# Kernel optimization log

Measured on AMD Instinct MI355X. Metric: run time of the kernel, lower is better.

## Reference

```python
import jax, jax.numpy as jnp
import numpy as np

D = 12  # grid size per axis (self.shape = [12,12,12])
BN_EPS = 1e-5


def _scatter(feats, idx, B):
    # feats: [N, C], idx: [N, 4] = (b, z, y, x). Coords are unique -> .set is exact.
    g = jnp.zeros((B, D, D, D, feats.shape[-1]), feats.dtype)
    return g.at[idx[:, 0], idx[:, 1], idx[:, 2], idx[:, 3]].set(feats)


def _subm_conv_bn_relu(feats, idx, B, W, b, gamma, beta):
    # Submanifold 3x3x3 conv == dense SAME conv on zero-filled grid, restricted
    # to the active sites (inactive neighbors contribute zero features).
    g = _scatter(feats, idx, B)  # [B, D, D, D, Cin]
    y = jax.lax.conv_general_dilated(
        g, W, window_strides=(1, 1, 1), padding='SAME',
        dimension_numbers=('NDHWC', 'DHWIO', 'NDHWC')) + b
    f = y[idx[:, 0], idx[:, 1], idx[:, 2], idx[:, 3]]  # gather active -> [N, Cout]
    # BatchNorm1d (training mode): biased batch stats over the N active points.
    mu = f.mean(axis=0)
    var = f.var(axis=0)
    f = (f - mu) * jax.lax.rsqrt(var + BN_EPS) * gamma + beta
    return jax.nn.relu(f)


def setup_inputs() -> dict:
    key = jax.random.key(0)
    B, per, Cin = 512, 864, 16
    N = B * per
    k_feat, k_coord, kp = jax.random.split(key, 3)
    # unique active voxels per batch element
    pkeys = jax.random.split(k_coord, B)
    lin = jax.vmap(lambda k: jax.random.permutation(k, D * D * D))(pkeys)[:, :per]  # [B, per]
    z, y, x = lin // (D * D), (lin // D) % D, lin % D
    bids = jnp.broadcast_to(jnp.arange(B)[:, None], (B, per))
    indices = jnp.stack([bids, z, y, x], axis=-1).reshape(N, 4).astype(jnp.int32)
    features = jax.random.normal(k_feat, (N, Cin), dtype=jnp.float32)
    ks = jax.random.split(kp, 6)
    inp = {
        'features': features, 'indices': indices, 'batch_size': B,
        'W0': jax.random.normal(ks[0], (3, 3, 3, Cin, 64), jnp.float32) * 0.05,
        'b0': jax.random.normal(ks[1], (64,), jnp.float32) * 0.05,
        'gamma0': jnp.ones((64,), jnp.float32), 'beta0': jnp.zeros((64,), jnp.float32),
        'W1': jax.random.normal(ks[2], (3, 3, 3, 64, 128), jnp.float32) * 0.05,
        'b1': jax.random.normal(ks[3], (128,), jnp.float32) * 0.05,
        'gamma1': jnp.ones((128,), jnp.float32), 'beta1': jnp.zeros((128,), jnp.float32),
        'W2': jax.random.normal(ks[4], (3, 3, 3, 128, 64), jnp.float32) * 0.05,
        'b2': jax.random.normal(ks[5], (64,), jnp.float32) * 0.05,
        'gamma2': jnp.ones((64,), jnp.float32), 'beta2': jnp.zeros((64,), jnp.float32),
    }
    return inp


def reference(features, indices, batch_size, W0, b0, gamma0, beta0,
              W1, b1, gamma1, beta1, W2, b2, gamma2, beta2):
    B = int(batch_size)
    f = _subm_conv_bn_relu(features, indices, B, W0, b0, gamma0, beta0)
    f = _subm_conv_bn_relu(f, indices, B, W1, b1, gamma1, beta1)
    f = _subm_conv_bn_relu(f, indices, B, W2, b2, gamma2, beta2)
    g = _scatter(f, indices, B)                 # [B, D, D, D, Cout]
    return jnp.transpose(g, (0, 4, 1, 2, 3))    # spconv .dense(): [B, C, D, H, W]
```

## Files before the change

kernel.cpp:

```cpp
#include <hip/hip_runtime.h>

#define DD 12
#define VOX 1728
#define BN_EPS 1e-5f
#define BATCH 512
#define PER 864
#define PERZ 865
#define NTOT (BATCH * PER)

typedef __attribute__((ext_vector_type(8))) short short8;
typedef __attribute__((ext_vector_type(4))) float f32x4;
typedef unsigned short u16;

__device__ inline u16 f2b(float f) {
    union { float f; unsigned u; } v; v.f = f;
    unsigned r = v.u + 0x7fffu + ((v.u >> 16) & 1u);
    return (u16)(r >> 16);
}
__device__ inline float b2f(u16 h) {
    union { unsigned u; float f; } v; v.u = ((unsigned)h) << 16;
    return v.f;
}
constexpr int ilog2(int v) { return v == 1 ? 0 : 1 + ilog2(v / 2); }

__device__ __forceinline__ void async_copy16(const void* g, void* l) {
    __builtin_amdgcn_global_load_lds(
        (const __attribute__((address_space(1))) void*)g,
        (__attribute__((address_space(3))) void*)l, 16, 0, 0);
}

template<int N> __device__ __forceinline__ void wait_vm() {
    if constexpr (N == 0)       asm volatile("s_waitcnt vmcnt(0)"  ::: "memory");
    else if constexpr (N == 8)  asm volatile("s_waitcnt vmcnt(8)"  ::: "memory");
    else if constexpr (N == 10) asm volatile("s_waitcnt vmcnt(10)" ::: "memory");
    else if constexpr (N == 12) asm volatile("s_waitcnt vmcnt(12)" ::: "memory");
    else if constexpr (N == 18) asm volatile("s_waitcnt vmcnt(18)" ::: "memory");
    else static_assert(N == 0, "unhandled vmcnt value");
}

__global__ void build_map_kernel(const int* __restrict__ idx, int* __restrict__ map, int N) {
    int p = blockIdx.x * blockDim.x + threadIdx.x;
    if (p >= N) return;
    const int4 v = ((const int4*)idx)[p];
    map[v.x * VOX + (v.y * DD + v.z) * DD + v.w] = p;
}

__global__ void build_nbr_kernel(const int* __restrict__ idx, const int* __restrict__ map,
                                 u16* __restrict__ nbr, int N) {
    int p = blockIdx.x * blockDim.x + threadIdx.x;
    if (p >= N) return;
    const int4 v = ((const int4*)idx)[p];
    const int base = v.x * VOX;
    const int lb = v.x * PER;
    #pragma unroll
    for (int nk = 0; nk < 27; nk++) {
        int dz = nk / 9 - 1, dy = (nk / 3) % 3 - 1, dx = nk % 3 - 1;
        int zz = v.y + dz, yy = v.z + dy, xx = v.w + dx;
        u16 out = PER;
        if (zz >= 0 && zz < DD && yy >= 0 && yy < DD && xx >= 0 && xx < DD) {
            int q = map[base + (zz * DD + yy) * DD + xx];
            if (q >= 0) out = (u16)(q - lb);
        }
        nbr[nk * N + p] = out;
    }
    #pragma unroll
    for (int nk = 27; nk < 32; nk++) nbr[nk * N + p] = PER;
}

__global__ void transpose_w_kernel(const float* __restrict__ W, u16* __restrict__ Wt,
                                   int K, int COUT, int Kpad) {
    int i = blockIdx.x * blockDim.x + threadIdx.x;
    if (i >= K * COUT) return;
    int n = i % COUT, k = i / COUT;
    Wt[(size_t)n * Kpad + k] = f2b(W[i]);
}

__global__ void zero_rows_kernel(u16* __restrict__ f, int CIN) {
    int t = blockIdx.x * blockDim.x + threadIdx.x;
    int e4 = CIN >> 2;
    if (t >= BATCH * e4) return;
    int b = t / e4, k = t - b * e4;
    ((ushort4*)f)[(size_t)(b * PERZ + PER) * e4 + k] = make_ushort4(0, 0, 0, 0);
}

__global__ void cast_bf16_kernel(const float* __restrict__ in, u16* __restrict__ out, int N4) {
    int i = blockIdx.x * blockDim.x + threadIdx.x;
    if (i >= N4) return;
    float4 v = ((const float4*)in)[i];
    int p = i >> 2, c4 = i & 3;
    int b = p / PER, r = p - b * PER;
    ushort4 o;
    o.x = f2b(v.x); o.y = f2b(v.y); o.z = f2b(v.z); o.w = f2b(v.w);
    ((ushort4*)out)[(size_t)(b * PERZ + r) * 4 + c4] = o;
}

template<int CIN, int COUT, int BM, int WM, int WN>
__global__ __launch_bounds__(256) void conv_mfma_kernel(
    const u16* __restrict__ fin,
    const u16* __restrict__ nbr,
    const u16* __restrict__ Wt,
    const float* __restrict__ bias,
    float* __restrict__ y,
    float* __restrict__ stats) {
    constexpr int Kpad   = (27 * CIN + 63) & ~63;
    constexpr int KSTEPS = Kpad / 64;
    constexpr int L2C    = ilog2(CIN);
    constexpr int BN     = WN * 64;
    constexpr int ASLOTS = BM / 32;
    constexpr int BSLOTS = BN / 32;
    constexpr int A_OFF  = BN * 128;
    constexpr int BUFB   = (BM + BN) * 128;
    static_assert(KSTEPS >= 3, "pipeline prologue needs >=3 K-steps");
    __shared__ char smem[2 * BUFB];

    const int perx = gridDim.x >> 3;
    const int bid = (blockIdx.x & 7) * perx + (blockIdx.x >> 3);
    const int p0 = bid * BM;

    const int tid = threadIdx.x;
    const int wave = tid >> 6, lane = tid & 63;
    const int wm = wave / WN, wn = wave % WN;
    const int lq = lane >> 4, lr = lane & 15;
    const int lrow = lane >> 3;
    const int kc_d = (lane & 7) ^ (lrow & 7);

    int qvoff[ASLOTS], gbase[ASLOTS];
    #pragma unroll
    for (int i = 0; i < ASLOTS; i++) {
        int m = (wave * ASLOTS + i) * 8 + lrow;
        int p = p0 + m;
        int b = p / PER;
        qvoff[i] = (((kc_d * 8) >> L2C) * NTOT + p) * 2;
        gbase[i] = b * PERZ * CIN + ((kc_d * 8) & (CIN - 1));
    }
    int bvoff[BSLOTS];
    #pragma unroll
    for (int j = 0; j < BSLOTS; j++)
        bvoff[j] = ((wave * BSLOTS + j) * 8 + lrow) * Kpad + kc_d * 8;

    int phs[2];
    phs[0] = ((0 + lq) ^ (lr & 7)) * 16;
    phs[1] = ((4 + lq) ^ (lr & 7)) * 16;
    const int aBase = A_OFF + (wm * 64 + lr) * 128;
    const int bBase = (wn * 64 + lr) * 128;

    const f32x4 fzero = {0.f, 0.f, 0.f, 0.f};
    f32x4 acc[4][4];
    #pragma unroll
    for (int i = 0; i < 4; i++)
        #pragma unroll
        for (int j = 0; j < 4; j++) acc[i][j] = fzero;

    u16 q[ASLOTS];
    auto loadQ = [&](int step) {
        int sQ = ((step * 64) >> L2C) * (NTOT * 2);
        #pragma unroll
        for (int i = 0; i < ASLOTS; i++)
            q[i] = *(const u16*)((const char*)nbr + qvoff[i] + sQ);
    };
    auto stage = [&](int step, int bo) {
        int sG = (step * 64) & (CIN - 1);
        const u16* fs = fin + sG;
        #pragma unroll
        for (int i = 0; i < ASLOTS; i++)
            async_copy16(fs + gbase[i] + ((int)q[i] << L2C),
                         smem + bo + A_OFF + (wave * ASLOTS + i) * 1024);
        const u16* wsrc = Wt + step * 64;
        #pragma unroll
        for (int j = 0; j < BSLOTS; j++)
            async_copy16(wsrc + bvoff[j], smem + bo + (wave * BSLOTS + j) * 1024);
    };

    loadQ(0);
    stage(0, 0);
    loadQ(1);

    #pragma unroll 1
    for (int kb = 0; kb < KSTEPS; kb++) {
        if (kb + 1 < KSTEPS) {
            stage(kb + 1, ((kb + 1) & 1) * BUFB);
            if (kb + 2 < KSTEPS) {
                loadQ(kb + 2);
                wait_vm<2 * ASLOTS + BSLOTS>();
            } else {
                wait_vm<ASLOTS + BSLOTS>();
            }
        } else {
            wait_vm<0>();
        }
        __builtin_amdgcn_s_barrier();

        const int so = (kb & 1) * BUFB;
        #pragma unroll
        for (int s = 0; s < 2; s++) {
            short8 af[4], bfr[4];
            #pragma unroll
            for (int i = 0; i < 4; i++)
                af[i] = *(const short8*)(smem + so + aBase + i * 2048 + phs[s]);
            #pragma unroll
            for (int j = 0; j < 4; j++)
                bfr[j] = *(const short8*)(smem + so + bBase + j * 2048 + phs[s]);
            #pragma unroll
            for (int i = 0; i < 4; i++)
                #pragma unroll
                for (int j = 0; j < 4; j++)
                    acc[i][j] = __builtin_amdgcn_mfma_f32_16x16x32_bf16(af[i], bfr[j], acc[i][j], 0, 0, 0);
        }
        asm volatile("s_waitcnt lgkmcnt(0)" ::: "memory");
        __builtin_amdgcn_s_barrier();
    }

    #pragma unroll
    for (int j = 0; j < 4; j++) {
        int col = wn * 64 + j * 16 + lr;
        float bv = bias[col];
        float s = 0.f, s2 = 0.f;
        #pragma unroll
        for (int i = 0; i < 4; i++) {
            int row0 = p0 + wm * 64 + i * 16 + lq * 4;
            #pragma unroll
            for (int r = 0; r < 4; r++) {
                float v = acc[i][j][r] + bv;
                y[(size_t)(row0 + r) * COUT + col] = v;
                s += v; s2 += v * v;
            }
        }
        s  += __shfl_down(s, 32);  s  += __shfl_down(s, 16);
        s2 += __shfl_down(s2, 32); s2 += __shfl_down(s2, 16);
        if (lane < 16) {
            atomicAdd(&stats[col], s);
            atomicAdd(&stats[COUT + col], s2);
        }
    }
}

template<int COUT>
__global__ void finalize_kernel(const float* __restrict__ stats, const float* __restrict__ gamma,
                                const float* __restrict__ beta, float* __restrict__ ss, int N) {
    int co = threadIdx.x;
    float inv_n = 1.f / (float)N;
    float mu  = stats[co] * inv_n;
    float var = stats[COUT + co] * inv_n - mu * mu;
    float sc  = gamma[co] * rsqrtf(var + BN_EPS);
    ss[co]        = sc;
    ss[COUT + co] = beta[co] - mu * sc;
}

template<int COUT>
__global__ void apply_kernel(const float* __restrict__ y, const float* __restrict__ ss,
                             u16* __restrict__ f, int total4) {
    int i = blockIdx.x * blockDim.x + threadIdx.x;
    if (i >= total4) return;
    constexpr int E4 = COUT / 4;
    float4 v = ((const float4*)y)[i];
    int p = i / E4, k = i - p * E4;
    int c0 = k * 4;
    int b = p / PER, r = p - b * PER;
    ushort4 o;
    float a;
    a = fmaf(v.x, ss[c0 + 0], ss[COUT + c0 + 0]); o.x = f2b(a > 0.f ? a : 0.f);
    a = fmaf(v.y, ss[c0 + 1], ss[COUT + c0 + 1]); o.y = f2b(a > 0.f ? a : 0.f);
    a = fmaf(v.z, ss[c0 + 2], ss[COUT + c0 + 2]); o.z = f2b(a > 0.f ? a : 0.f);
    a = fmaf(v.w, ss[c0 + 3], ss[COUT + c0 + 3]); o.w = f2b(a > 0.f ? a : 0.f);
    ((ushort4*)f)[(size_t)(b * PERZ + r) * E4 + k] = o;
}

__global__ void output_kernel(const u16* __restrict__ f, const int* __restrict__ map,
                              float* __restrict__ out, int total) {
    int i = blockIdx.x * blockDim.x + threadIdx.x;
    if (i >= total) return;
    int voxel = i % VOX;
    int bc    = i / VOX;
    int c = bc & 63;
    int b = bc >> 6;
    int p = map[b * VOX + voxel];
    float v = 0.f;
    if (p >= 0) {
        int r = p - b * PER;
        v = b2f(f[(size_t)(b * PERZ + r) * 64 + c]);
    }
    out[i] = v;
}

extern "C" void kernel_launch(void* const* d_in, const int* in_sizes, int n_in,
                              void* d_out, int out_size, void* d_ws, size_t ws_size,
                              hipStream_t stream) {
    const float* feats = (const float*)d_in[0];
    const int*   idx   = (const int*)  d_in[1];
    const float* W0 = (const float*)d_in[3];
    const float* b0 = (const float*)d_in[4];
    const float* g0 = (const float*)d_in[5];
    const float* e0 = (const float*)d_in[6];
    const float* W1 = (const float*)d_in[7];
    const float* b1 = (const float*)d_in[8];
    const float* g1 = (const float*)d_in[9];
    const float* e1 = (const float*)d_in[10];
    const float* W2 = (const float*)d_in[11];
    const float* b2 = (const float*)d_in[12];
    const float* g2 = (const float*)d_in[13];
    const float* e2 = (const float*)d_in[14];

    const int N = in_sizes[0] / 16;

    char* ws = (char*)d_ws;
    size_t off = 0;
    auto alloc = [&](size_t bytes) { void* p = ws + off; off = (off + bytes + 255) & ~(size_t)255; return p; };
    int*   map   = (int*)  alloc((size_t)BATCH * VOX * 4);
    float* stats = (float*)alloc(3 * 256 * 4);
    float* ss    = (float*)alloc(3 * 256 * 4);
    u16*   nbr   = (u16*)  alloc((size_t)N * 32 * 2);
    u16*   wt0   = (u16*)  alloc((size_t)64  * 448  * 2);
    u16*   wt1   = (u16*)  alloc((size_t)128 * 1728 * 2);
    u16*   wt2   = (u16*)  alloc((size_t)64  * 3456 * 2);
    u16*   fbuf  = (u16*)  alloc((size_t)BATCH * PERZ * 128 * 2);
    float* y = (float*)d_out;

    hipMemsetAsync(map,   0xFF, (size_t)BATCH * VOX * 4, stream);
    hipMemsetAsync(stats, 0,    3 * 256 * 4, stream);
    hipMemsetAsync(wt0,   0,    (size_t)64 * 448 * 2, stream);
    build_map_kernel<<<(N + 255) / 256, 256, 0, stream>>>(idx, map, N);
    build_nbr_kernel<<<(N + 255) / 256, 256, 0, stream>>>(idx, map, nbr, N);
    transpose_w_kernel<<<(432  * 64  + 255) / 256, 256, 0, stream>>>(W0, wt0, 432,  64,  448);
    transpose_w_kernel<<<(1728 * 128 + 255) / 256, 256, 0, stream>>>(W1, wt1, 1728, 128, 1728);
    transpose_w_kernel<<<(3456 * 64  + 255) / 256, 256, 0, stream>>>(W2, wt2, 3456, 64,  3456);

    zero_rows_kernel<<<(BATCH * 4 + 255) / 256, 256, 0, stream>>>(fbuf, 16);
    cast_bf16_kernel<<<(N * 4 + 255) / 256, 256, 0, stream>>>(feats, fbuf, N * 4);
    conv_mfma_kernel<16, 64, 256, 4, 1><<<N / 256, 256, 0, stream>>>(fbuf, nbr, wt0, b0, y, stats + 0);
    finalize_kernel<64><<<1, 64, 0, stream>>>(stats + 0, g0, e0, ss + 0, N);
    zero_rows_kernel<<<(BATCH * 16 + 255) / 256, 256, 0, stream>>>(fbuf, 64);
    apply_kernel<64><<<(N * 16 + 255) / 256, 256, 0, stream>>>(y, ss + 0, fbuf, N * 16);

    conv_mfma_kernel<64, 128, 128, 2, 2><<<N / 128, 256, 0, stream>>>(fbuf, nbr, wt1, b1, y, stats + 256);
    finalize_kernel<128><<<1, 128, 0, stream>>>(stats + 256, g1, e1, ss + 256, N);
    zero_rows_kernel<<<(BATCH * 32 + 255) / 256, 256, 0, stream>>>(fbuf, 128);
    apply_kernel<128><<<(N * 32 + 255) / 256, 256, 0, stream>>>(y, ss + 256, fbuf, N * 32);

    conv_mfma_kernel<128, 64, 256, 4, 1><<<N / 256, 256, 0, stream>>>(fbuf, nbr, wt2, b2, y, stats + 512);
    finalize_kernel<64><<<1, 64, 0, stream>>>(stats + 512, g2, e2, ss + 512, N);
    zero_rows_kernel<<<(BATCH * 16 + 255) / 256, 256, 0, stream>>>(fbuf, 64);
    apply_kernel<64><<<(N * 16 + 255) / 256, 256, 0, stream>>>(y, ss + 512, fbuf, N * 16);

    output_kernel<<<(out_size + 255) / 256, 256, 0, stream>>>(fbuf, map, (float*)d_out, out_size);
}
```

Before: 1.358 ms.

## Load weight fragments directly into registers from pre-packed MFMA layout, skipping LDS

Weights are pre-packed into a layout where each lane's MFMA B fragment is one contiguous 16-byte load. The conv kernel now reads B straight from global memory (L2-resident) into double-buffered registers instead of staging it through LDS. This halves LDS traffic and shrinks the shared memory footprint, which may raise occupancy. The cost is more VGPRs (16 short8 buffers) and more in-flight vector memory ops that each step has to wait on.

After: 1.561 ms. 1.15x slower.

```diff
diff --git a/kernel.cpp b/kernel.cpp
--- a/kernel.cpp
+++ b/kernel.cpp
@@ -31,10 +31,9 @@
 
 template<int N> __device__ __forceinline__ void wait_vm() {
     if constexpr (N == 0)       asm volatile("s_waitcnt vmcnt(0)"  ::: "memory");
-    else if constexpr (N == 8)  asm volatile("s_waitcnt vmcnt(8)"  ::: "memory");
-    else if constexpr (N == 10) asm volatile("s_waitcnt vmcnt(10)" ::: "memory");
     else if constexpr (N == 12) asm volatile("s_waitcnt vmcnt(12)" ::: "memory");
-    else if constexpr (N == 18) asm volatile("s_waitcnt vmcnt(18)" ::: "memory");
+    else if constexpr (N == 16) asm volatile("s_waitcnt vmcnt(16)" ::: "memory");
+    else if constexpr (N == 24) asm volatile("s_waitcnt vmcnt(24)" ::: "memory");
     else static_assert(N == 0, "unhandled vmcnt value");
 }
 
@@ -67,12 +66,28 @@
     for (int nk = 27; nk < 32; nk++) nbr[nk * N + p] = PER;
 }
 
-__global__ void transpose_w_kernel(const float* __restrict__ W, u16* __restrict__ Wt,
-                                   int K, int COUT, int Kpad) {
-    int i = blockIdx.x * blockDim.x + threadIdx.x;
-    if (i >= K * COUT) return;
-    int n = i % COUT, k = i / COUT;
-    Wt[(size_t)n * Kpad + k] = f2b(W[i]);
+template<int CIN, int COUT>
+__global__ void pack_w_kernel(const float* __restrict__ W, u16* __restrict__ Wp) {
+    constexpr int K = 27 * CIN;
+    constexpr int KSTEPS = ((K + 63) & ~63) / 64;
+    constexpr int NG = COUT / 64;
+    int t = blockIdx.x * blockDim.x + threadIdx.x;
+    if (t >= KSTEPS * NG * 8 * 64) return;
+    int lane = t & 63;
+    int sj   = (t >> 6) & 7;
+    int gg   = t >> 9;
+    int g = gg % NG, step = gg / NG;
+    int col = g * 64 + (sj & 3) * 16 + (lane & 15);
+    int k0  = step * 64 + (sj >> 2) * 32 + (lane >> 4) * 8;
+    short8 o;
+    #pragma unroll
+    for (int e = 0; e < 8; e++) {
+        int k = k0 + e;
+        u16 val = 0;
+        if (k < K) val = f2b(W[(size_t)k * COUT + col]);
+        ((u16*)&o)[e] = val;
+    }
+    *(short8*)(Wp + (size_t)t * 8) = o;
 }
 
 __global__ void zero_rows_kernel(u16* __restrict__ f, int CIN) {
@@ -98,18 +113,16 @@
 __global__ __launch_bounds__(256) void conv_mfma_kernel(
     const u16* __restrict__ fin,
     const u16* __restrict__ nbr,
-    const u16* __restrict__ Wt,
+    const u16* __restrict__ Wp,
     const float* __restrict__ bias,
     float* __restrict__ y,
     float* __restrict__ stats) {
     constexpr int Kpad   = (27 * CIN + 63) & ~63;
     constexpr int KSTEPS = Kpad / 64;
     constexpr int L2C    = ilog2(CIN);
-    constexpr int BN     = WN * 64;
+    constexpr int NG     = COUT / 64;
     constexpr int ASLOTS = BM / 32;
-    constexpr int BSLOTS = BN / 32;
-    constexpr int A_OFF  = BN * 128;
-    constexpr int BUFB   = (BM + BN) * 128;
+    constexpr int BUFB   = BM * 128;
     static_assert(KSTEPS >= 3, "pipeline prologue needs >=3 K-steps");
     __shared__ char smem[2 * BUFB];
 
@@ -133,16 +146,11 @@
         qvoff[i] = (((kc_d * 8) >> L2C) * NTOT + p) * 2;
         gbase[i] = b * PERZ * CIN + ((kc_d * 8) & (CIN - 1));
     }
-    int bvoff[BSLOTS];
-    #pragma unroll
-    for (int j = 0; j < BSLOTS; j++)
-        bvoff[j] = ((wave * BSLOTS + j) * 8 + lrow) * Kpad + kc_d * 8;
 
     int phs[2];
     phs[0] = ((0 + lq) ^ (lr & 7)) * 16;
     phs[1] = ((4 + lq) ^ (lr & 7)) * 16;
-    const int aBase = A_OFF + (wm * 64 + lr) * 128;
-    const int bBase = (wn * 64 + lr) * 128;
+    const int aBase = (wm * 64 + lr) * 128;
 
     const f32x4 fzero = {0.f, 0.f, 0.f, 0.f};
     f32x4 acc[4][4];
@@ -164,50 +172,60 @@
         #pragma unroll
         for (int i = 0; i < ASLOTS; i++)
             async_copy16(fs + gbase[i] + ((int)q[i] << L2C),
-                         smem + bo + A_OFF + (wave * ASLOTS + i) * 1024);
-        const u16* wsrc = Wt + step * 64;
-        #pragma unroll
-        for (int j = 0; j < BSLOTS; j++)
-            async_copy16(wsrc + bvoff[j], smem + bo + (wave * BSLOTS + j) * 1024);
-    };
-
-    loadQ(0);
-    stage(0, 0);
-    loadQ(1);
-
-    #pragma unroll 1
-    for (int kb = 0; kb < KSTEPS; kb++) {
-        if (kb + 1 < KSTEPS) {
-            stage(kb + 1, ((kb + 1) & 1) * BUFB);
-            if (kb + 2 < KSTEPS) {
-                loadQ(kb + 2);
-                wait_vm<2 * ASLOTS + BSLOTS>();
-            } else {
-                wait_vm<ASLOTS + BSLOTS>();
-            }
-        } else {
-            wait_vm<0>();
-        }
-        __builtin_amdgcn_s_barrier();
-
-        const int so = (kb & 1) * BUFB;
+                         smem + bo + (wave * ASLOTS + i) * 1024);
+    };
+    const char* wpB = (const char*)Wp + (size_t)wn * 8 * 1024 + (size_t)lane * 16;
+    auto loadB = [&](int step, short8 (&bb)[8]) {
+        const char* src = wpB + (size_t)step * (NG * 8 * 1024);
+        #pragma unroll
+        for (int sj = 0; sj < 8; sj++)
+            bb[sj] = *(const short8*)(src + sj * 1024);
+    };
+    auto compute = [&](const short8 (&bb)[8], int so) {
         #pragma unroll
         for (int s = 0; s < 2; s++) {
-            short8 af[4], bfr[4];
+            short8 af[4];
             #pragma unroll
             for (int i = 0; i < 4; i++)
                 af[i] = *(const short8*)(smem + so + aBase + i * 2048 + phs[s]);
             #pragma unroll
-            for (int j = 0; j < 4; j++)
-                bfr[j] = *(const short8*)(smem + so + bBase + j * 2048 + phs[s]);
-            #pragma unroll
             for (int i = 0; i < 4; i++)
                 #pragma unroll
                 for (int j = 0; j < 4; j++)
-                    acc[i][j] = __builtin_amdgcn_mfma_f32_16x16x32_bf16(af[i], bfr[j], acc[i][j], 0, 0, 0);
-        }
+                    acc[i][j] = __builtin_amdgcn_mfma_f32_16x16x32_bf16(af[i], bb[s * 4 + j], acc[i][j], 0, 0, 0);
+        }
+    };
+
+    auto step_body = [&](int kb, short8 (&bC)[8], short8 (&bN)[8]) {
+        if (kb + 1 < KSTEPS) {
+            stage(kb + 1, ((kb + 1) & 1) * BUFB);
+            loadB(kb + 1, bN);
+            if (kb + 2 < KSTEPS) {
+                loadQ(kb + 2);
+                wait_vm<2 * ASLOTS + 8>();
+            } else {
+                wait_vm<ASLOTS + 8>();
+            }
+        } else {
+            wait_vm<0>();
+        }
+        __builtin_amdgcn_s_barrier();
+        compute(bC, (kb & 1) * BUFB);
         asm volatile("s_waitcnt lgkmcnt(0)" ::: "memory");
         __builtin_amdgcn_s_barrier();
+    };
+
+    short8 bX[8], bY[8];
+    loadQ(0);
+    stage(0, 0);
+    loadB(0, bX);
+    loadQ(1);
+
+    #pragma unroll 1
+    for (int kb = 0; kb < KSTEPS; kb += 2) {
+        step_body(kb, bX, bY);
+        if (kb + 1 < KSTEPS)
+            step_body(kb + 1, bY, bX);
     }
 
     #pragma unroll
@@ -309,20 +327,19 @@
     float* stats = (float*)alloc(3 * 256 * 4);
     float* ss    = (float*)alloc(3 * 256 * 4);
     u16*   nbr   = (u16*)  alloc((size_t)N * 32 * 2);
-    u16*   wt0   = (u16*)  alloc((size_t)64  * 448  * 2);
-    u16*   wt1   = (u16*)  alloc((size_t)128 * 1728 * 2);
-    u16*   wt2   = (u16*)  alloc((size_t)64  * 3456 * 2);
+    u16*   wt0   = (u16*)  alloc((size_t)7  * 1 * 512 * 16);
+    u16*   wt1   = (u16*)  alloc((size_t)27 * 2 * 512 * 16);
+    u16*   wt2   = (u16*)  alloc((size_t)54 * 1 * 512 * 16);
     u16*   fbuf  = (u16*)  alloc((size_t)BATCH * PERZ * 128 * 2);
     float* y = (float*)d_out;
 
     hipMemsetAsync(map,   0xFF, (size_t)BATCH * VOX * 4, stream);
     hipMemsetAsync(stats, 0,    3 * 256 * 4, stream);
-    hipMemsetAsync(wt0,   0,    (size_t)64 * 448 * 2, stream);
     build_map_kernel<<<(N + 255) / 256, 256, 0, stream>>>(idx, map, N);
     build_nbr_kernel<<<(N + 255) / 256, 256, 0, stream>>>(idx, map, nbr, N);
-    transpose_w_kernel<<<(432  * 64  + 255) / 256, 256, 0, stream>>>(W0, wt0, 432,  64,  448);
-    transpose_w_kernel<<<(1728 * 128 + 255) / 256, 256, 0, stream>>>(W1, wt1, 1728, 128, 1728);
-    transpose_w_kernel<<<(3456 * 64  + 255) / 256, 256, 0, stream>>>(W2, wt2, 3456, 64,  3456);
+    pack_w_kernel<16,  64 ><<<(7  * 1 * 512 + 255) / 256, 256, 0, stream>>>(W0, wt0);
+    pack_w_kernel<64,  128><<<(27 * 2 * 512 + 255) / 256, 256, 0, stream>>>(W1, wt1);
+    pack_w_kernel<128, 64 ><<<(54 * 1 * 512 + 255) / 256, 256, 0, stream>>>(W2, wt2);
 
     zero_rows_kernel<<<(BATCH * 4 + 255) / 256, 256, 0, stream>>>(fbuf, 16);
     cast_bf16_kernel<<<(N * 4 + 255) / 256, 256, 0, stream>>>(feats, fbuf, N * 4);
```

## Fuse final BN/ReLU into dense output scatter and fold zero-row padding into cast/apply

Applied to the files above, without the earlier changes.

Removes the separate zero_rows launches by having the cast and apply kernels cover padded rows and write zeros there. Conv priority is raised around the MFMA block with s_setprio. When the workspace allows, the last conv writes to a separate buffer and a new fused kernel applies BN+ReLU while transposing through shared memory into the dense NCDHW output. This skips the final bf16 round trip and the strided output gather, at the cost of extra workspace and a fallback path.

Measured after the change: 1.193 ms. -12.1%, faster.

```diff
diff --git a/kernel.cpp b/kernel.cpp
--- a/kernel.cpp
+++ b/kernel.cpp
@@ -75,23 +75,17 @@
     Wt[(size_t)n * Kpad + k] = f2b(W[i]);
 }
 
-__global__ void zero_rows_kernel(u16* __restrict__ f, int CIN) {
-    int t = blockIdx.x * blockDim.x + threadIdx.x;
-    int e4 = CIN >> 2;
-    if (t >= BATCH * e4) return;
-    int b = t / e4, k = t - b * e4;
-    ((ushort4*)f)[(size_t)(b * PERZ + PER) * e4 + k] = make_ushort4(0, 0, 0, 0);
-}
-
-__global__ void cast_bf16_kernel(const float* __restrict__ in, u16* __restrict__ out, int N4) {
+__global__ void cast_bf16_kernel(const float* __restrict__ in, u16* __restrict__ out, int total4) {
     int i = blockIdx.x * blockDim.x + threadIdx.x;
-    if (i >= N4) return;
-    float4 v = ((const float4*)in)[i];
+    if (i >= total4) return;
     int p = i >> 2, c4 = i & 3;
-    int b = p / PER, r = p - b * PER;
-    ushort4 o;
-    o.x = f2b(v.x); o.y = f2b(v.y); o.z = f2b(v.z); o.w = f2b(v.w);
-    ((ushort4*)out)[(size_t)(b * PERZ + r) * 4 + c4] = o;
+    int b = p / PERZ, r = p - b * PERZ;
+    ushort4 o = make_ushort4(0, 0, 0, 0);
+    if (r < PER) {
+        float4 v = ((const float4*)in)[(size_t)(b * PER + r) * 4 + c4];
+        o.x = f2b(v.x); o.y = f2b(v.y); o.z = f2b(v.z); o.w = f2b(v.w);
+    }
+    ((ushort4*)out)[i] = o;
 }
 
 template<int CIN, int COUT, int BM, int WM, int WN>
@@ -191,6 +185,7 @@
         __builtin_amdgcn_s_barrier();
 
         const int so = (kb & 1) * BUFB;
+        __builtin_amdgcn_s_setprio(1);
         #pragma unroll
         for (int s = 0; s < 2; s++) {
             short8 af[4], bfr[4];
@@ -206,6 +201,7 @@
                 for (int j = 0; j < 4; j++)
                     acc[i][j] = __builtin_amdgcn_mfma_f32_16x16x32_bf16(af[i], bfr[j], acc[i][j], 0, 0, 0);
         }
+        __builtin_amdgcn_s_setprio(0);
         asm volatile("s_waitcnt lgkmcnt(0)" ::: "memory");
         __builtin_amdgcn_s_barrier();
     }
@@ -252,17 +248,19 @@
     int i = blockIdx.x * blockDim.x + threadIdx.x;
     if (i >= total4) return;
     constexpr int E4 = COUT / 4;
-    float4 v = ((const float4*)y)[i];
     int p = i / E4, k = i - p * E4;
-    int c0 = k * 4;
-    int b = p / PER, r = p - b * PER;
-    ushort4 o;
-    float a;
-    a = fmaf(v.x, ss[c0 + 0], ss[COUT + c0 + 0]); o.x = f2b(a > 0.f ? a : 0.f);
-    a = fmaf(v.y, ss[c0 + 1], ss[COUT + c0 + 1]); o.y = f2b(a > 0.f ? a : 0.f);
-    a = fmaf(v.z, ss[c0 + 2], ss[COUT + c0 + 2]); o.z = f2b(a > 0.f ? a : 0.f);
-    a = fmaf(v.w, ss[c0 + 3], ss[COUT + c0 + 3]); o.w = f2b(a > 0.f ? a : 0.f);
-    ((ushort4*)f)[(size_t)(b * PERZ + r) * E4 + k] = o;
+    int b = p / PERZ, r = p - b * PERZ;
+    ushort4 o = make_ushort4(0, 0, 0, 0);
+    if (r < PER) {
+        float4 v = ((const float4*)y)[(size_t)(b * PER + r) * E4 + k];
+        int c0 = k * 4;
+        float a;
+        a = fmaf(v.x, ss[c0 + 0], ss[COUT + c0 + 0]); o.x = f2b(a > 0.f ? a : 0.f);
+        a = fmaf(v.y, ss[c0 + 1], ss[COUT + c0 + 1]); o.y = f2b(a > 0.f ? a : 0.f);
+        a = fmaf(v.z, ss[c0 + 2], ss[COUT + c0 + 2]); o.z = f2b(a > 0.f ? a : 0.f);
+        a = fmaf(v.w, ss[c0 + 3], ss[COUT + c0 + 3]); o.w = f2b(a > 0.f ? a : 0.f);
+    }
+    ((ushort4*)f)[i] = o;
 }
 
 __global__ void output_kernel(const u16* __restrict__ f, const int* __restrict__ map,
@@ -280,6 +278,34 @@
         v = b2f(f[(size_t)(b * PERZ + r) * 64 + c]);
     }
     out[i] = v;
+}
+
+__global__ void output_fused_kernel(const float* __restrict__ y, const float* __restrict__ ss,
+                                    const int* __restrict__ map, float* __restrict__ out) {
+    __shared__ float tile[64][65];
+    __shared__ int   prow[64];
+    const int chunk = blockIdx.x;
+    const int b  = chunk / (VOX / 64);
+    const int v0 = (chunk % (VOX / 64)) * 64;
+    const int t = threadIdx.x;
+    if (t < 64) prow[t] = map[b * VOX + v0 + t];
+    __syncthreads();
+    const int c = t & 63;
+    const float sc = ss[c], sh = ss[64 + c];
+    for (int v = t >> 6; v < 64; v += 4) {
+        int p = prow[v];
+        float val = 0.f;
+        if (p >= 0) {
+            float a = fmaf(y[(size_t)p * 64 + c], sc, sh);
+            val = a > 0.f ? a : 0.f;
+        }
+        tile[v][c] = val;
+    }
+    __syncthreads();
+    const int vv = t & 63;
+    #pragma unroll
+    for (int cc = t >> 6; cc < 64; cc += 4)
+        out[(size_t)(b * 64 + cc) * VOX + v0 + vv] = tile[vv][cc];
 }
 
 extern "C" void kernel_launch(void* const* d_in, const int* in_sizes, int n_in,
@@ -315,6 +341,10 @@
     u16*   fbuf  = (u16*)  alloc((size_t)BATCH * PERZ * 128 * 2);
     float* y = (float*)d_out;
 
+    const size_t y3_bytes = (size_t)N * 64 * 4;
+    float* y3 = nullptr;
+    if (off + y3_bytes <= ws_size) y3 = (float*)alloc(y3_bytes);
+
     hipMemsetAsync(map,   0xFF, (size_t)BATCH * VOX * 4, stream);
     hipMemsetAsync(stats, 0,    3 * 256 * 4, stream);
     hipMemsetAsync(wt0,   0,    (size_t)64 * 448 * 2, stream);
@@ -324,22 +354,23 @@
     transpose_w_kernel<<<(1728 * 128 + 255) / 256, 256, 0, stream>>>(W1, wt1, 1728, 128, 1728);
     transpose_w_kernel<<<(3456 * 64  + 255) / 256, 256, 0, stream>>>(W2, wt2, 3456, 64,  3456);
 
-    zero_rows_kernel<<<(BATCH * 4 + 255) / 256, 256, 0, stream>>>(fbuf, 16);
-    cast_bf16_kernel<<<(N * 4 + 255) / 256, 256, 0, stream>>>(feats, fbuf, N * 4);
+    cast_bf16_kernel<<<(BATCH * PERZ * 4 + 255) / 256, 256, 0, stream>>>(feats, fbuf, BATCH * PERZ * 4);
     conv_mfma_kernel<16, 64, 256, 4, 1><<<N / 256, 256, 0, stream>>>(fbuf, nbr, wt0, b0, y, stats + 0);
     finalize_kernel<64><<<1, 64, 0, stream>>>(stats + 0, g0, e0, ss + 0, N);
-    zero_rows_kernel<<<(BATCH * 16 + 255) / 256, 256, 0, stream>>>(fbuf, 64);
-    apply_kernel<64><<<(N * 16 + 255) / 256, 256, 0, stream>>>(y, ss + 0, fbuf, N * 16);
+    apply_kernel<64><<<(BATCH * PERZ * 16 + 255) / 256, 256, 0, stream>>>(y, ss + 0, fbuf, BATCH * PERZ * 16);
 
     conv_mfma_kernel<64, 128, 128, 2, 2><<<N / 128, 256, 0, stream>>>(fbuf, nbr, wt1, b1, y, stats + 256);
     finalize_kernel<128><<<1, 128, 0, stream>>>(stats + 256, g1, e1, ss + 256, N);
-    zero_rows_kernel<<<(BATCH * 32 + 255) / 256, 256, 0, stream>>>(fbuf, 128);
-    apply_kernel<128><<<(N * 32 + 255) / 256, 256, 0, stream>>>(y, ss + 256, fbuf, N * 32);
-
-    conv_mfma_kernel<128, 64, 256, 4, 1><<<N / 256, 256, 0, stream>>>(fbuf, nbr, wt2, b2, y, stats + 512);
+    apply_kernel<128><<<(BATCH * PERZ * 32 + 255) / 256, 256, 0, stream>>>(y, ss + 256, fbuf, BATCH * PERZ * 32);
+
+    float* yL3 = y3 ? y3 : y;
+    conv_mfma_kernel<128, 64, 256, 4, 1><<<N / 256, 256, 0, stream>>>(fbuf, nbr, wt2, b2, yL3, stats + 512);
     finalize_kernel<64><<<1, 64, 0, stream>>>(stats + 512, g2, e2, ss + 512, N);
-    zero_rows_kernel<<<(BATCH * 16 + 255) / 256, 256, 0, stream>>>(fbuf, 64);
-    apply_kernel<64><<<(N * 16 + 255) / 256, 256, 0, stream>>>(y, ss + 512, fbuf, N * 16);
-
-    output_kernel<<<(out_size + 255) / 256, 256, 0, stream>>>(fbuf, map, (float*)d_out, out_size);
-}
+
+    if (y3) {
+        output_fused_kernel<<<BATCH * (VOX / 64), 256, 0, stream>>>(y3, ss + 512, map, (float*)d_out);
+    } else {
+        apply_kernel<64><<<(BATCH * PERZ * 16 + 255) / 256, 256, 0, stream>>>(y, ss + 512, fbuf, BATCH * PERZ * 16);
+        output_kernel<<<(out_size + 255) / 256, 256, 0, stream>>>(fbuf, map, (float*)d_out, out_size);
+    }
+}
```
